# Optimization experiments

Hardware: AMD Instinct MI355X
Metric: run time of the kernel (lower is better)

The kernel has to match this reference:

```python
import jax, jax.numpy as jnp
import numpy as np

N_NODES = 50000
N_EDGES = 800000
D_FEAT = 64
THETA = [0.5, 0.3, 0.15, 0.05]  # polynomial filter coefficients, k = len(THETA)


def setup_inputs() -> dict:
    key = jax.random.key(0)
    k1, k2, k3 = jax.random.split(key, 3)
    feat = jax.random.normal(k1, (N_NODES, D_FEAT), dtype=jnp.float32)
    src = jax.random.randint(k2, (N_EDGES,), 0, N_NODES)  # A[src, dst] = 1
    dst = jax.random.randint(k3, (N_EDGES,), 0, N_NODES)
    return {"feat": feat, "src": src, "dst": dst}


def reference(feat, src, dst):
    # normalize_adj: D^{-1/2} A^T D^{-1/2} with D = rowsum(A) (inf -> 0 for isolated nodes).
    n = feat.shape[0]
    deg = jax.ops.segment_sum(jnp.ones(src.shape, dtype=feat.dtype), src, num_segments=n)
    d_inv_sqrt = jnp.where(deg > 0, jax.lax.rsqrt(jnp.maximum(deg, 1.0)), jnp.zeros_like(deg))
    # norm[i, j] = d_i^{-1/2} A[j, i] d_j^{-1/2}; edge (src=j, dst=i) carries weight
    w = d_inv_sqrt[src] * d_inv_sqrt[dst]  # [E]

    def spmm(x):
        # (A_norm @ x)[i] = sum over edges with dst==i of w_e * x[src_e]
        return jax.ops.segment_sum(w[:, None] * x[src], dst, num_segments=n)

    # Original loop: h = theta[0]*(A@f); for k>=1: f = A@f; h += theta[k]*f.
    # Note theta[0] and theta[1] both scale A@f0 (feat is not updated before h init),
    # so we fold them together and avoid recomputing the first SpMM.
    x = spmm(feat)  # A @ f0, shared by the k=0 and k=1 terms
    h = (THETA[0] + THETA[1]) * x
    for k in range(2, len(THETA)):
        x = spmm(x)
        h = h + THETA[k] * x
    return h
```

## Files before the change

kernel.cpp:

```cpp
#include <hip/hip_runtime.h>
#include <hip/hip_bf16.h>

#define N_NODES 50000
#define N_EDGES 800000
#define D_FEAT  64
#define NW      12500
#define G_SRC   64
#define G_DST   256
#define CONV_NB 128
#define FILL_NB 64
#define HB      512
#define SCAN_B  256
#define SCAN_NBLK ((NW + SCAN_B - 1) / SCAN_B)
#define CAP     48


__device__ __forceinline__ float bflo(unsigned u) { return __uint_as_float(u << 16); }
__device__ __forceinline__ float bfhi(unsigned u) { return __uint_as_float(u & 0xFFFF0000u); }
__device__ __forceinline__ unsigned pack_bf16(float a, float b) {
    __hip_bfloat16 x = __float2bfloat16(a), y = __float2bfloat16(b);
    unsigned short ux = *reinterpret_cast<unsigned short*>(&x);
    unsigned short uy = *reinterpret_cast<unsigned short*>(&y);
    return (unsigned)ux | ((unsigned)uy << 16);
}


__global__ void hist_cv_kernel(const int* __restrict__ src, const int* __restrict__ dst,
                               unsigned* __restrict__ psrc_p, unsigned* __restrict__ pdst_p,
                               const float* __restrict__ feat, unsigned* __restrict__ featbf,
                               int2* __restrict__ csr2, int nE) {
    int t = threadIdx.x;
    int b = blockIdx.x;
    if (b >= G_SRC + G_DST + CONV_NB) {
        int fb = b - (G_SRC + G_DST + CONV_NB);
        uint4* c4 = (uint4*)csr2;
        const int n4 = N_NODES * CAP / 2;
        const int nthr = FILL_NB * HB;
        uint4 z = make_uint4(0u, 0u, 0u, 0u);
        for (int i = fb * HB + t; i < n4; i += nthr) c4[i] = z;
        return;
    }
    if (b >= G_SRC + G_DST) {
        int cb = b - (G_SRC + G_DST);
        const float4* f4 = (const float4*)feat;
        uint2* fb2 = (uint2*)featbf;
        const int nthr = CONV_NB * HB;
        for (int i = cb * HB + t; i < N_NODES * 16; i += nthr) {
            float4 v = f4[i];
            fb2[i] = make_uint2(pack_bf16(v.x, v.y), pack_bf16(v.z, v.w));
        }
        return;
    }
    __shared__ unsigned bins[NW];
    for (int i = t; i < NW; i += HB) bins[i] = 0;
    __syncthreads();
    bool is_src = (b < G_SRC);
    int g = is_src ? b : (b - G_SRC);
    int nstr = is_src ? G_SRC : G_DST;
    const int4* k4 = (const int4*)(is_src ? src : dst);
    int nE4 = nE >> 2;
    for (int q = g * HB + t; q < nE4; q += nstr * HB) {
        int4 kv = k4[q];
        atomicAdd(&bins[kv.x >> 2], 1u << (8 * (kv.x & 3)));
        atomicAdd(&bins[kv.y >> 2], 1u << (8 * (kv.y & 3)));
        atomicAdd(&bins[kv.z >> 2], 1u << (8 * (kv.z & 3)));
        atomicAdd(&bins[kv.w >> 2], 1u << (8 * (kv.w & 3)));
    }
    __syncthreads();
    unsigned* p = (is_src ? psrc_p : pdst_p) + g * NW;
    for (int i = t; i < NW; i += HB) p[i] = bins[i];
}

__global__ void scanA_kernel(const unsigned* __restrict__ pdst_p, const unsigned* __restrict__ psrc_p,
                             unsigned* __restrict__ gbase_p, float* __restrict__ dinv) {
    int w = blockIdx.x * SCAN_B + threadIdx.x;
    if (w >= NW) return;
    unsigned td = 0;
    #pragma unroll 16
    for (int g = 0; g < G_DST; g++) {
        gbase_p[g * NW + w] = td;
        td += pdst_p[g * NW + w];
    }
    unsigned ts = 0;
    #pragma unroll 16
    for (int g = 0; g < G_SRC; g++) ts += psrc_p[g * NW + w];
    unsigned d0 = ts & 255u, d1 = (ts >> 8) & 255u, d2 = (ts >> 16) & 255u, d3 = ts >> 24;
    float4 dv;
    dv.x = d0 ? rsqrtf((float)d0) : 0.0f;
    dv.y = d1 ? rsqrtf((float)d1) : 0.0f;
    dv.z = d2 ? rsqrtf((float)d2) : 0.0f;
    dv.w = d3 ? rsqrtf((float)d3) : 0.0f;
    ((float4*)dinv)[w] = dv;
}

__global__ void scatter_kernel(const int* __restrict__ src, const int* __restrict__ dst,
                               const unsigned* __restrict__ gbase_p, const float* __restrict__ dinv,
                               int2* __restrict__ csr2, int nE) {
    __shared__ unsigned cur[NW];
    int t = threadIdx.x;
    int g = blockIdx.x;
    const unsigned* gb = gbase_p + (size_t)g * NW;
    for (int i = t; i < NW; i += HB) cur[i] = gb[i];
    __syncthreads();
    const int4* s4 = (const int4*)src;
    const int4* d4 = (const int4*)dst;
    int nE4 = nE >> 2;
    for (int q = g * HB + t; q < nE4; q += G_DST * HB) {
        int4 sv = s4[q];
        int4 dv = d4[q];
        {
            int k = dv.x; int sh = 8 * (k & 3);
            unsigned old = atomicAdd(&cur[k >> 2], 1u << sh);
            csr2[(size_t)k * CAP + ((old >> sh) & 255u)] = make_int2(sv.x, __float_as_int(dinv[sv.x]));
        }
        {
            int k = dv.y; int sh = 8 * (k & 3);
            unsigned old = atomicAdd(&cur[k >> 2], 1u << sh);
            csr2[(size_t)k * CAP + ((old >> sh) & 255u)] = make_int2(sv.y, __float_as_int(dinv[sv.y]));
        }
        {
            int k = dv.z; int sh = 8 * (k & 3);
            unsigned old = atomicAdd(&cur[k >> 2], 1u << sh);
            csr2[(size_t)k * CAP + ((old >> sh) & 255u)] = make_int2(sv.z, __float_as_int(dinv[sv.z]));
        }
        {
            int k = dv.w; int sh = 8 * (k & 3);
            unsigned old = atomicAdd(&cur[k >> 2], 1u << sh);
            csr2[(size_t)k * CAP + ((old >> sh) & 255u)] = make_int2(sv.w, __float_as_int(dinv[sv.w]));
        }
    }
}


struct Acc8 { float a0, a1, a2, a3, a4, a5, a6, a7; };

__device__ __forceinline__ Acc8 spmm_gather(int i, const int2* __restrict__ csr2,
                                            const unsigned* __restrict__ x,
                                            int eg, int c8) {
    const int2* row = csr2 + (size_t)i * CAP;
    const uint4* x4 = (const uint4*)x;
    int2 sw0 = row[eg];
    int2 sw1 = row[eg + 8];
    int2 sw2 = row[eg + 16];
    int2 sw3 = row[eg + 24];
    int2 sw4 = row[eg + 32];
    int2 sw5 = row[eg + 40];
    uint4 r0 = x4[(size_t)sw0.x * 8 + c8];
    uint4 r1 = x4[(size_t)sw1.x * 8 + c8];
    uint4 r2 = x4[(size_t)sw2.x * 8 + c8];
    uint4 r3 = x4[(size_t)sw3.x * 8 + c8];
    uint4 r4 = x4[(size_t)sw4.x * 8 + c8];
    uint4 r5 = x4[(size_t)sw5.x * 8 + c8];
    float w0 = __int_as_float(sw0.y), w1 = __int_as_float(sw1.y);
    float w2 = __int_as_float(sw2.y), w3 = __int_as_float(sw3.y);
    float w4 = __int_as_float(sw4.y), w5 = __int_as_float(sw5.y);
    float a0, a1, a2, a3, a4, a5, a6, a7;
    a0  = w0 * bflo(r0.x) + w1 * bflo(r1.x) + w2 * bflo(r2.x);
    a1  = w0 * bfhi(r0.x) + w1 * bfhi(r1.x) + w2 * bfhi(r2.x);
    a2  = w0 * bflo(r0.y) + w1 * bflo(r1.y) + w2 * bflo(r2.y);
    a3  = w0 * bfhi(r0.y) + w1 * bfhi(r1.y) + w2 * bfhi(r2.y);
    a4  = w0 * bflo(r0.z) + w1 * bflo(r1.z) + w2 * bflo(r2.z);
    a5  = w0 * bfhi(r0.z) + w1 * bfhi(r1.z) + w2 * bfhi(r2.z);
    a6  = w0 * bflo(r0.w) + w1 * bflo(r1.w) + w2 * bflo(r2.w);
    a7  = w0 * bfhi(r0.w) + w1 * bfhi(r1.w) + w2 * bfhi(r2.w);
    a0 += w3 * bflo(r3.x) + w4 * bflo(r4.x) + w5 * bflo(r5.x);
    a1 += w3 * bfhi(r3.x) + w4 * bfhi(r4.x) + w5 * bfhi(r5.x);
    a2 += w3 * bflo(r3.y) + w4 * bflo(r4.y) + w5 * bflo(r5.y);
    a3 += w3 * bfhi(r3.y) + w4 * bfhi(r4.y) + w5 * bfhi(r5.y);
    a4 += w3 * bflo(r3.z) + w4 * bflo(r4.z) + w5 * bflo(r5.z);
    a5 += w3 * bfhi(r3.z) + w4 * bfhi(r4.z) + w5 * bfhi(r5.z);
    a6 += w3 * bflo(r3.w) + w4 * bflo(r4.w) + w5 * bflo(r5.w);
    a7 += w3 * bfhi(r3.w) + w4 * bfhi(r4.w) + w5 * bfhi(r5.w);
    #pragma unroll
    for (int d = 8; d <= 32; d <<= 1) {
        a0 += __shfl_xor(a0, d); a1 += __shfl_xor(a1, d);
        a2 += __shfl_xor(a2, d); a3 += __shfl_xor(a3, d);
        a4 += __shfl_xor(a4, d); a5 += __shfl_xor(a5, d);
        a6 += __shfl_xor(a6, d); a7 += __shfl_xor(a7, d);
    }
    Acc8 r = {a0, a1, a2, a3, a4, a5, a6, a7};
    return r;
}

__global__ void spmm_mid_kernel(const int2* __restrict__ csr2, const float* __restrict__ dinv,
                                const unsigned* __restrict__ x, unsigned* __restrict__ y) {
    int i = (blockIdx.x * blockDim.x + threadIdx.x) >> 6;
    if (i >= N_NODES) return;
    int lane = threadIdx.x & 63;
    Acc8 A = spmm_gather(i, csr2, x, lane >> 3, lane & 7);
    if (lane < 8) {
        int c8 = lane & 7;
        float di = dinv[i];
        uint4 p;
        p.x = pack_bf16(A.a0 * di, A.a1 * di);
        p.y = pack_bf16(A.a2 * di, A.a3 * di);
        p.z = pack_bf16(A.a4 * di, A.a5 * di);
        p.w = pack_bf16(A.a6 * di, A.a7 * di);
        ((uint4*)y)[(size_t)i * 8 + c8] = p;
    }
}

__global__ void spmm_final_kernel(const int2* __restrict__ csr2, const float* __restrict__ dinv,
                                  const unsigned* __restrict__ x1, const unsigned* __restrict__ x2,
                                  float* __restrict__ h) {
    int i = (blockIdx.x * blockDim.x + threadIdx.x) >> 6;
    if (i >= N_NODES) return;
    int lane = threadIdx.x & 63;
    Acc8 A = spmm_gather(i, csr2, x2, lane >> 3, lane & 7);
    if (lane < 8) {
        int c8 = lane & 7;
        float di = dinv[i] * 0.05f;
        uint4 u1 = ((const uint4*)x1)[(size_t)i * 8 + c8];
        uint4 u2 = ((const uint4*)x2)[(size_t)i * 8 + c8];
        float4 o0, o1;
        o0.x = 0.8f * bflo(u1.x) + 0.15f * bflo(u2.x) + di * A.a0;
        o0.y = 0.8f * bfhi(u1.x) + 0.15f * bfhi(u2.x) + di * A.a1;
        o0.z = 0.8f * bflo(u1.y) + 0.15f * bflo(u2.y) + di * A.a2;
        o0.w = 0.8f * bfhi(u1.y) + 0.15f * bfhi(u2.y) + di * A.a3;
        o1.x = 0.8f * bflo(u1.z) + 0.15f * bflo(u2.z) + di * A.a4;
        o1.y = 0.8f * bfhi(u1.z) + 0.15f * bfhi(u2.z) + di * A.a5;
        o1.z = 0.8f * bflo(u1.w) + 0.15f * bflo(u2.w) + di * A.a6;
        o1.w = 0.8f * bfhi(u1.w) + 0.15f * bfhi(u2.w) + di * A.a7;
        float4* h4 = (float4*)h;
        size_t hbase = (size_t)i * 16 + (size_t)c8 * 2;
        h4[hbase] = o0;
        h4[hbase + 1] = o1;
    }
}


extern "C" void kernel_launch(void* const* d_in, const int* in_sizes, int n_in,
                              void* d_out, int out_size, void* d_ws, size_t ws_size,
                              hipStream_t stream) {
    const float* feat = (const float*)d_in[0];
    const int*   src  = (const int*)d_in[1];
    const int*   dst  = (const int*)d_in[2];
    float* h = (float*)d_out;

    char* ws = (char*)d_ws;
    unsigned* psrc_p   = (unsigned*)(ws);
    unsigned* pdst_p   = (unsigned*)(ws +  3200000u);
    unsigned* gbase_p  = (unsigned*)(ws + 16000000u);
    float*    dinv     = (float*)   (ws + 28800000u);
    int2*     csr2     = (int2*)    (ws + 29000192u);
    unsigned* featbf   = (unsigned*)(ws + 48200192u);
    unsigned* bufA     = (unsigned*)(ws + 54600192u);
    unsigned* bufB     = (unsigned*)(ws + 61000192u);

    const int nE = N_EDGES;
    const int B = 256;

    hist_cv_kernel<<<G_SRC + G_DST + CONV_NB + FILL_NB, HB, 0, stream>>>(
        src, dst, psrc_p, pdst_p, feat, featbf, csr2, nE);

    scanA_kernel<<<SCAN_NBLK, SCAN_B, 0, stream>>>(pdst_p, psrc_p, gbase_p, dinv);

    scatter_kernel<<<G_DST, HB, 0, stream>>>(src, dst, gbase_p, dinv, csr2, nE);

    const int spmmGrid = (N_NODES * 64 + B - 1) / B;
    spmm_mid_kernel<<<spmmGrid, B, 0, stream>>>(csr2, dinv, featbf, bufA);
    spmm_mid_kernel<<<spmmGrid, B, 0, stream>>>(csr2, dinv, bufA, bufB);
    spmm_final_kernel<<<spmmGrid, B, 0, stream>>>(csr2, dinv, bufA, bufB, h);
}
```

Baseline: 170.4 us.

## Split bf16 features into two 32-column panels and drop per-edge weights from CSR

Feature buffers are stored as two column panels of 32 bf16 values each, and every SpMM runs twice, once per panel. This shrinks the gathered working set per pass so it fits better in cache. The CSR now holds only source indices, padded with a dedicated zero row instead of index 0, and the source normalisation is read from dinv at gather time. A 64-lane wave now covers 16 edge slots times 4 column chunks with one more shuffle stage, at the cost of twice as many kernel launches and CSR row reads.

```diff
diff --git a/kernel.cpp b/kernel.cpp
--- a/kernel.cpp
+++ b/kernel.cpp
@@ -13,6 +13,8 @@
 #define SCAN_B  256
 #define SCAN_NBLK ((NW + SCAN_B - 1) / SCAN_B)
 #define CAP     48
+#define ZROW    50000
+#define PANEL_U32 800032
 
 
 __device__ __forceinline__ float bflo(unsigned u) { return __uint_as_float(u << 16); }
@@ -28,26 +30,36 @@
 __global__ void hist_cv_kernel(const int* __restrict__ src, const int* __restrict__ dst,
                                unsigned* __restrict__ psrc_p, unsigned* __restrict__ pdst_p,
                                const float* __restrict__ feat, unsigned* __restrict__ featbf,
-                               int2* __restrict__ csr2, int nE) {
+                               unsigned* __restrict__ bufA, unsigned* __restrict__ bufB,
+                               int* __restrict__ csr, int nE) {
     int t = threadIdx.x;
     int b = blockIdx.x;
     if (b >= G_SRC + G_DST + CONV_NB) {
         int fb = b - (G_SRC + G_DST + CONV_NB);
-        uint4* c4 = (uint4*)csr2;
-        const int n4 = N_NODES * CAP / 2;
+        uint4* c4 = (uint4*)csr;
+        const int n4 = N_NODES * CAP / 4;
         const int nthr = FILL_NB * HB;
-        uint4 z = make_uint4(0u, 0u, 0u, 0u);
-        for (int i = fb * HB + t; i < n4; i += nthr) c4[i] = z;
+        uint4 zv = make_uint4(ZROW, ZROW, ZROW, ZROW);
+        for (int i = fb * HB + t; i < n4; i += nthr) c4[i] = zv;
+        if (fb == 0 && t < 96) {
+            int buf = t >> 5;
+            int pan = (t >> 4) & 1;
+            int word = t & 15;
+            unsigned* base = (buf == 0 ? featbf : (buf == 1 ? bufA : bufB)) + (size_t)pan * PANEL_U32;
+            base[(size_t)ZROW * 16 + word] = 0u;
+        }
         return;
     }
     if (b >= G_SRC + G_DST) {
         int cb = b - (G_SRC + G_DST);
         const float4* f4 = (const float4*)feat;
-        uint2* fb2 = (uint2*)featbf;
         const int nthr = CONV_NB * HB;
         for (int i = cb * HB + t; i < N_NODES * 16; i += nthr) {
             float4 v = f4[i];
-            fb2[i] = make_uint2(pack_bf16(v.x, v.y), pack_bf16(v.z, v.w));
+            int node = i >> 4, col4 = i & 15;
+            int pan = col4 >> 3, off = col4 & 7;
+            uint2* pb = (uint2*)(featbf + (size_t)pan * PANEL_U32);
+            pb[(size_t)node * 8 + off] = make_uint2(pack_bf16(v.x, v.y), pack_bf16(v.z, v.w));
         }
         return;
     }
@@ -74,6 +86,7 @@
 __global__ void scanA_kernel(const unsigned* __restrict__ pdst_p, const unsigned* __restrict__ psrc_p,
                              unsigned* __restrict__ gbase_p, float* __restrict__ dinv) {
     int w = blockIdx.x * SCAN_B + threadIdx.x;
+    if (blockIdx.x == 0 && threadIdx.x == 0) dinv[ZROW] = 0.0f;
     if (w >= NW) return;
     unsigned td = 0;
     #pragma unroll 16
@@ -94,8 +107,8 @@
 }
 
 __global__ void scatter_kernel(const int* __restrict__ src, const int* __restrict__ dst,
-                               const unsigned* __restrict__ gbase_p, const float* __restrict__ dinv,
-                               int2* __restrict__ csr2, int nE) {
+                               const unsigned* __restrict__ gbase_p,
+                               int* __restrict__ csr, int nE) {
     __shared__ unsigned cur[NW];
     int t = threadIdx.x;
     int g = blockIdx.x;
@@ -111,22 +124,22 @@
         {
             int k = dv.x; int sh = 8 * (k & 3);
             unsigned old = atomicAdd(&cur[k >> 2], 1u << sh);
-            csr2[(size_t)k * CAP + ((old >> sh) & 255u)] = make_int2(sv.x, __float_as_int(dinv[sv.x]));
+            csr[(size_t)k * CAP + ((old >> sh) & 255u)] = sv.x;
         }
         {
             int k = dv.y; int sh = 8 * (k & 3);
             unsigned old = atomicAdd(&cur[k >> 2], 1u << sh);
-            csr2[(size_t)k * CAP + ((old >> sh) & 255u)] = make_int2(sv.y, __float_as_int(dinv[sv.y]));
+            csr[(size_t)k * CAP + ((old >> sh) & 255u)] = sv.y;
         }
         {
             int k = dv.z; int sh = 8 * (k & 3);
             unsigned old = atomicAdd(&cur[k >> 2], 1u << sh);
-            csr2[(size_t)k * CAP + ((old >> sh) & 255u)] = make_int2(sv.z, __float_as_int(dinv[sv.z]));
+            csr[(size_t)k * CAP + ((old >> sh) & 255u)] = sv.z;
         }
         {
             int k = dv.w; int sh = 8 * (k & 3);
             unsigned old = atomicAdd(&cur[k >> 2], 1u << sh);
-            csr2[(size_t)k * CAP + ((old >> sh) & 255u)] = make_int2(sv.w, __float_as_int(dinv[sv.w]));
+            csr[(size_t)k * CAP + ((old >> sh) & 255u)] = sv.w;
         }
     }
 }
@@ -134,45 +147,30 @@
 
 struct Acc8 { float a0, a1, a2, a3, a4, a5, a6, a7; };
 
-__device__ __forceinline__ Acc8 spmm_gather(int i, const int2* __restrict__ csr2,
-                                            const unsigned* __restrict__ x,
-                                            int eg, int c8) {
-    const int2* row = csr2 + (size_t)i * CAP;
-    const uint4* x4 = (const uint4*)x;
-    int2 sw0 = row[eg];
-    int2 sw1 = row[eg + 8];
-    int2 sw2 = row[eg + 16];
-    int2 sw3 = row[eg + 24];
-    int2 sw4 = row[eg + 32];
-    int2 sw5 = row[eg + 40];
-    uint4 r0 = x4[(size_t)sw0.x * 8 + c8];
-    uint4 r1 = x4[(size_t)sw1.x * 8 + c8];
-    uint4 r2 = x4[(size_t)sw2.x * 8 + c8];
-    uint4 r3 = x4[(size_t)sw3.x * 8 + c8];
-    uint4 r4 = x4[(size_t)sw4.x * 8 + c8];
-    uint4 r5 = x4[(size_t)sw5.x * 8 + c8];
-    float w0 = __int_as_float(sw0.y), w1 = __int_as_float(sw1.y);
-    float w2 = __int_as_float(sw2.y), w3 = __int_as_float(sw3.y);
-    float w4 = __int_as_float(sw4.y), w5 = __int_as_float(sw5.y);
+__device__ __forceinline__ Acc8 gather_panel(int i, const int* __restrict__ csr,
+                                             const float* __restrict__ dinv,
+                                             const unsigned* __restrict__ xp,
+                                             int eg, int c4) {
+    const int* row = csr + (size_t)i * CAP;
+    const uint4* x4 = (const uint4*)xp;
+    int s0 = row[eg];
+    int s1 = row[eg + 16];
+    int s2 = row[eg + 32];
+    float d0 = dinv[s0], d1 = dinv[s1], d2 = dinv[s2];
+    uint4 r0 = x4[(size_t)s0 * 4 + c4];
+    uint4 r1 = x4[(size_t)s1 * 4 + c4];
+    uint4 r2 = x4[(size_t)s2 * 4 + c4];
     float a0, a1, a2, a3, a4, a5, a6, a7;
-    a0  = w0 * bflo(r0.x) + w1 * bflo(r1.x) + w2 * bflo(r2.x);
-    a1  = w0 * bfhi(r0.x) + w1 * bfhi(r1.x) + w2 * bfhi(r2.x);
-    a2  = w0 * bflo(r0.y) + w1 * bflo(r1.y) + w2 * bflo(r2.y);
-    a3  = w0 * bfhi(r0.y) + w1 * bfhi(r1.y) + w2 * bfhi(r2.y);
-    a4  = w0 * bflo(r0.z) + w1 * bflo(r1.z) + w2 * bflo(r2.z);
-    a5  = w0 * bfhi(r0.z) + w1 * bfhi(r1.z) + w2 * bfhi(r2.z);
-    a6  = w0 * bflo(r0.w) + w1 * bflo(r1.w) + w2 * bflo(r2.w);
-    a7  = w0 * bfhi(r0.w) + w1 * bfhi(r1.w) + w2 * bfhi(r2.w);
-    a0 += w3 * bflo(r3.x) + w4 * bflo(r4.x) + w5 * bflo(r5.x);
-    a1 += w3 * bfhi(r3.x) + w4 * bfhi(r4.x) + w5 * bfhi(r5.x);
-    a2 += w3 * bflo(r3.y) + w4 * bflo(r4.y) + w5 * bflo(r5.y);
-    a3 += w3 * bfhi(r3.y) + w4 * bfhi(r4.y) + w5 * bfhi(r5.y);
-    a4 += w3 * bflo(r3.z) + w4 * bflo(r4.z) + w5 * bflo(r5.z);
-    a5 += w3 * bfhi(r3.z) + w4 * bfhi(r4.z) + w5 * bfhi(r5.z);
-    a6 += w3 * bflo(r3.w) + w4 * bflo(r4.w) + w5 * bflo(r5.w);
-    a7 += w3 * bfhi(r3.w) + w4 * bfhi(r4.w) + w5 * bfhi(r5.w);
+    a0 = d0 * bflo(r0.x) + d1 * bflo(r1.x) + d2 * bflo(r2.x);
+    a1 = d0 * bfhi(r0.x) + d1 * bfhi(r1.x) + d2 * bfhi(r2.x);
+    a2 = d0 * bflo(r0.y) + d1 * bflo(r1.y) + d2 * bflo(r2.y);
+    a3 = d0 * bfhi(r0.y) + d1 * bfhi(r1.y) + d2 * bfhi(r2.y);
+    a4 = d0 * bflo(r0.z) + d1 * bflo(r1.z) + d2 * bflo(r2.z);
+    a5 = d0 * bfhi(r0.z) + d1 * bfhi(r1.z) + d2 * bfhi(r2.z);
+    a6 = d0 * bflo(r0.w) + d1 * bflo(r1.w) + d2 * bflo(r2.w);
+    a7 = d0 * bfhi(r0.w) + d1 * bfhi(r1.w) + d2 * bfhi(r2.w);
     #pragma unroll
-    for (int d = 8; d <= 32; d <<= 1) {
+    for (int d = 4; d <= 32; d <<= 1) {
         a0 += __shfl_xor(a0, d); a1 += __shfl_xor(a1, d);
         a2 += __shfl_xor(a2, d); a3 += __shfl_xor(a3, d);
         a4 += __shfl_xor(a4, d); a5 += __shfl_xor(a5, d);
@@ -182,36 +180,35 @@
     return r;
 }
 
-__global__ void spmm_mid_kernel(const int2* __restrict__ csr2, const float* __restrict__ dinv,
-                                const unsigned* __restrict__ x, unsigned* __restrict__ y) {
+__global__ void spmm_mid_kernel(const int* __restrict__ csr, const float* __restrict__ dinv,
+                                const unsigned* __restrict__ xp, unsigned* __restrict__ yp) {
     int i = (blockIdx.x * blockDim.x + threadIdx.x) >> 6;
     if (i >= N_NODES) return;
     int lane = threadIdx.x & 63;
-    Acc8 A = spmm_gather(i, csr2, x, lane >> 3, lane & 7);
-    if (lane < 8) {
-        int c8 = lane & 7;
+    Acc8 A = gather_panel(i, csr, dinv, xp, lane >> 2, lane & 3);
+    if (lane < 4) {
         float di = dinv[i];
         uint4 p;
         p.x = pack_bf16(A.a0 * di, A.a1 * di);
         p.y = pack_bf16(A.a2 * di, A.a3 * di);
         p.z = pack_bf16(A.a4 * di, A.a5 * di);
         p.w = pack_bf16(A.a6 * di, A.a7 * di);
-        ((uint4*)y)[(size_t)i * 8 + c8] = p;
-    }
-}
-
-__global__ void spmm_final_kernel(const int2* __restrict__ csr2, const float* __restrict__ dinv,
-                                  const unsigned* __restrict__ x1, const unsigned* __restrict__ x2,
-                                  float* __restrict__ h) {
+        ((uint4*)yp)[(size_t)i * 4 + lane] = p;
+    }
+}
+
+__global__ void spmm_final_kernel(const int* __restrict__ csr, const float* __restrict__ dinv,
+                                  const unsigned* __restrict__ x1p, const unsigned* __restrict__ x2p,
+                                  float* __restrict__ h, int colbase) {
     int i = (blockIdx.x * blockDim.x + threadIdx.x) >> 6;
     if (i >= N_NODES) return;
     int lane = threadIdx.x & 63;
-    Acc8 A = spmm_gather(i, csr2, x2, lane >> 3, lane & 7);
-    if (lane < 8) {
-        int c8 = lane & 7;
+    Acc8 A = gather_panel(i, csr, dinv, x2p, lane >> 2, lane & 3);
+    if (lane < 4) {
+        int c4 = lane;
         float di = dinv[i] * 0.05f;
-        uint4 u1 = ((const uint4*)x1)[(size_t)i * 8 + c8];
-        uint4 u2 = ((const uint4*)x2)[(size_t)i * 8 + c8];
+        uint4 u1 = ((const uint4*)x1p)[(size_t)i * 4 + c4];
+        uint4 u2 = ((const uint4*)x2p)[(size_t)i * 4 + c4];
         float4 o0, o1;
         o0.x = 0.8f * bflo(u1.x) + 0.15f * bflo(u2.x) + di * A.a0;
         o0.y = 0.8f * bfhi(u1.x) + 0.15f * bfhi(u2.x) + di * A.a1;
@@ -221,10 +218,9 @@
         o1.y = 0.8f * bfhi(u1.z) + 0.15f * bfhi(u2.z) + di * A.a5;
         o1.z = 0.8f * bflo(u1.w) + 0.15f * bflo(u2.w) + di * A.a6;
         o1.w = 0.8f * bfhi(u1.w) + 0.15f * bfhi(u2.w) + di * A.a7;
-        float4* h4 = (float4*)h;
-        size_t hbase = (size_t)i * 16 + (size_t)c8 * 2;
-        h4[hbase] = o0;
-        h4[hbase + 1] = o1;
+        float4* h4 = (float4*)(h + (size_t)i * 64 + colbase + c4 * 8);
+        h4[0] = o0;
+        h4[1] = o1;
     }
 }
 
@@ -242,23 +238,30 @@
     unsigned* pdst_p   = (unsigned*)(ws +  3200000u);
     unsigned* gbase_p  = (unsigned*)(ws + 16000000u);
     float*    dinv     = (float*)   (ws + 28800000u);
-    int2*     csr2     = (int2*)    (ws + 29000192u);
-    unsigned* featbf   = (unsigned*)(ws + 48200192u);
-    unsigned* bufA     = (unsigned*)(ws + 54600192u);
-    unsigned* bufB     = (unsigned*)(ws + 61000192u);
+    int*      csr      = (int*)     (ws + 29000192u);
+    unsigned* featbf   = (unsigned*)(ws + 38600192u);
+    unsigned* bufA     = (unsigned*)(ws + 45000448u);
+    unsigned* bufB     = (unsigned*)(ws + 51400704u);
 
     const int nE = N_EDGES;
     const int B = 256;
 
+    unsigned* featA = featbf;               unsigned* featB = featbf + PANEL_U32;
+    unsigned* bufAA = bufA;                 unsigned* bufAB = bufA + PANEL_U32;
+    unsigned* bufBA = bufB;                 unsigned* bufBB = bufB + PANEL_U32;
+
     hist_cv_kernel<<<G_SRC + G_DST + CONV_NB + FILL_NB, HB, 0, stream>>>(
-        src, dst, psrc_p, pdst_p, feat, featbf, csr2, nE);
+        src, dst, psrc_p, pdst_p, feat, featbf, bufA, bufB, csr, nE);
 
     scanA_kernel<<<SCAN_NBLK, SCAN_B, 0, stream>>>(pdst_p, psrc_p, gbase_p, dinv);
 
-    scatter_kernel<<<G_DST, HB, 0, stream>>>(src, dst, gbase_p, dinv, csr2, nE);
+    scatter_kernel<<<G_DST, HB, 0, stream>>>(src, dst, gbase_p, csr, nE);
 
     const int spmmGrid = (N_NODES * 64 + B - 1) / B;
-    spmm_mid_kernel<<<spmmGrid, B, 0, stream>>>(csr2, dinv, featbf, bufA);
-    spmm_mid_kernel<<<spmmGrid, B, 0, stream>>>(csr2, dinv, bufA, bufB);
-    spmm_final_kernel<<<spmmGrid, B, 0, stream>>>(csr2, dinv, bufA, bufB, h);
-}
+    spmm_mid_kernel<<<spmmGrid, B, 0, stream>>>(csr, dinv, featA, bufAA);
+    spmm_mid_kernel<<<spmmGrid, B, 0, stream>>>(csr, dinv, featB, bufAB);
+    spmm_mid_kernel<<<spmmGrid, B, 0, stream>>>(csr, dinv, bufAA, bufBA);
+    spmm_mid_kernel<<<spmmGrid, B, 0, stream>>>(csr, dinv, bufAB, bufBB);
+    spmm_final_kernel<<<spmmGrid, B, 0, stream>>>(csr, dinv, bufAA, bufBA, h, 0);
+    spmm_final_kernel<<<spmmGrid, B, 0, stream>>>(csr, dinv, bufAB, bufBB, h, 32);
+}
```

Result: slower. 217.1 us (+27.4%).
